# Kernel optimization log

Hardware: AMD Instinct MI355X
Metric: run time of the kernel (lower is better)

## Reference

```python
import jax, jax.numpy as jnp
import numpy as np

B, N, E = 4, 2048, 512
H, DK, DV = 8, 64, 64
QKV_OUT = H * (2 * DK + DV)  # 1536


def setup_inputs() -> dict:
    key = jax.random.key(0)
    ks = jax.random.split(key, 5)
    s_in = 1.0 / np.sqrt(E)
    s_o = 1.0 / np.sqrt(H * DV)
    x = jax.random.normal(ks[0], (B, N, E), dtype=jnp.float32)
    W_qkv = jax.random.uniform(ks[1], (E, QKV_OUT), jnp.float32, -s_in, s_in)
    b_qkv = jax.random.uniform(ks[2], (QKV_OUT,), jnp.float32, -s_in, s_in)
    W_o = jax.random.uniform(ks[3], (H * DV, E), jnp.float32, -s_o, s_o)
    b_o = jax.random.uniform(ks[4], (E,), jnp.float32, -s_o, s_o)
    return {"x": x, "W_qkv": W_qkv, "b_qkv": b_qkv, "W_o": W_o, "b_o": b_o}


def reference(x, W_qkv, b_qkv, W_o, b_o):
    scale = DK ** (-0.5)
    qkv = x @ W_qkv + b_qkv                      # [B, N, H*(2dk+dv)]
    # Faithful to torch: raw view (B, H, N, 2dk+dv), NOT a head-split transpose.
    qkv = qkv.reshape(B, H, N, 2 * DK + DV)
    q = qkv[..., :DK]
    k = qkv[..., DK:2 * DK]
    v = qkv[..., 2 * DK:]
    # Faithful bug: qk /= scale with scale = dk^-0.5 -> multiply by sqrt(dk).
    qk = jnp.einsum('bhnd,bhmd->bhnm', q, k) / scale   # [B, H, N, N]
    attn = jax.nn.softmax(qk, axis=-1)
    y = jnp.einsum('bhnm,bhmd->bhnd', attn, v)         # [B, H, N, dv]
    y = y.reshape(B, N, H * DV)
    return y @ W_o + b_o
```

## Files before the change

kernel.cpp:

```cpp
#include <hip/hip_runtime.h>
#include <hip/hip_bf16.h>
#include <math.h>


typedef __attribute__((ext_vector_type(8))) short bf16x8;
typedef __attribute__((ext_vector_type(4))) float f32x4;

#define MFMA16(a, b, c) __builtin_amdgcn_mfma_f32_16x16x32_bf16((a), (b), (c), 0, 0, 0)

__device__ __forceinline__ ushort f2bf_rne(float f) {
  union { float f; unsigned u; } v; v.f = f;
  return (ushort)((v.u + 0x7fffu + ((v.u >> 16) & 1u)) >> 16);
}
__device__ __forceinline__ float bf2f(ushort h) {
  union { float f; unsigned u; } v; v.u = ((unsigned)h) << 16; return v.f;
}
__device__ __forceinline__ void split2(float f, ushort& hi, ushort& lo) {
  union { float f; unsigned u; } v; v.f = f;
  hi = (ushort)(v.u >> 16);
  union { float f; unsigned u; } r; r.f = f - bf2f(hi);
  lo = (ushort)(r.u >> 16);
}

typedef __attribute__((address_space(3))) unsigned int lds_uint;
typedef const __attribute__((address_space(1))) unsigned int glob_uint;
__device__ __forceinline__ void gl_lds16(const ushort* g, short* l) {
  __builtin_amdgcn_global_load_lds((glob_uint*)g, (lds_uint*)l, 16, 0, 0);
}

template <bool ROOMY>
__global__ __launch_bounds__(256) void cvt_k(const float* __restrict__ wqkv,
                                             const float* __restrict__ wo,
                                             const float* __restrict__ x,
                                             ushort* __restrict__ wT_hi,
                                             ushort* __restrict__ wT_lo,
                                             ushort* __restrict__ woT,
                                             ushort* __restrict__ xh,
                                             ushort* __restrict__ xl)
{
  const int gid = blockIdx.x * 256 + threadIdx.x;
  if (gid < 786432) {
    const int c   = gid / 49152;
    const int rem = gid - c * 49152;
    const int n   = rem >> 5;
    const int k   = c * 32 + (rem & 31);
    ushort hi, lo; split2(wqkv[(size_t)k * 1536 + n], hi, lo);
    wT_hi[gid] = hi; wT_lo[gid] = lo;
  } else if (gid < 1048576) {
    const int g = gid - 786432;
    const int n = g >> 9, k = g & 511;
    woT[g] = f2bf_rne(wo[(size_t)k * 512 + n]);
  } else if (ROOMY) {
    const int g = gid - 1048576;
    float4 v = ((const float4*)x)[g];
    ushort4 hh, ll;
    split2(v.x, hh.x, ll.x); split2(v.y, hh.y, ll.y);
    split2(v.z, hh.z, ll.z); split2(v.w, hh.w, ll.w);
    ((ushort4*)xh)[g] = hh;
    ((ushort4*)xl)[g] = ll;
  }
}

template <bool PRECVT>
__global__ __launch_bounds__(256) void qkv_gemm_k(
    const float* __restrict__ x,
    const ushort* __restrict__ xh, const ushort* __restrict__ xl,
    const ushort* __restrict__ wT_hi, const ushort* __restrict__ wT_lo,
    const float* __restrict__ bqkv,
    ushort* __restrict__ q_hi, ushort* __restrict__ q_lo,
    ushort* __restrict__ k_hi, ushort* __restrict__ k_lo,
    ushort* __restrict__ v_nat)
{
  const int i = blockIdx.x, j = i >> 3;
  const int tmb = (i & 7) * 8 + (j & 7);
  const int tn  = j >> 3;
  const int tid = threadIdx.x, lane = tid & 63, w = tid >> 6;
  const int col16 = lane & 15, quad = lane >> 4;
  const int wr = w >> 1, wc = w & 1;

  __shared__ short sbuf[16384];

  const int wl   = w * 1024 + lane * 8;
  const int ldsw = w * 1024;
  const ushort* shp = wT_hi + (size_t)tn * 4096 + wl;
  const ushort* slp = wT_lo + (size_t)tn * 4096 + wl;

  const float*  axf[4];
  const ushort *axh[4], *axl[4];
#pragma unroll
  for (int rt = 0; rt < 4; ++rt) {
    const size_t rowoff = (size_t)(tmb * 128 + wr * 64 + rt * 16 + col16) * 512 + quad * 8;
    axf[rt] = x  + rowoff;
    axh[rt] = xh + rowoff;
    axl[rt] = xl + rowoff;
  }

  f32x4 acc[4][4];
#pragma unroll
  for (int rt = 0; rt < 4; ++rt)
#pragma unroll
    for (int ct = 0; ct < 4; ++ct) acc[rt][ct] = (f32x4){0.f, 0.f, 0.f, 0.f};

  gl_lds16(shp,       sbuf + ldsw);
  gl_lds16(shp + 512, sbuf + ldsw + 512);
  gl_lds16(slp,       sbuf + 8192 + ldsw);
  gl_lds16(slp + 512, sbuf + 8192 + ldsw + 512);
  __syncthreads();

  int buf = 0;
#pragma unroll
  for (int c = 0; c < 16; ++c) {
    if (c < 15) {
      const size_t co = (size_t)(c + 1) * 49152;
      const int nb = (buf ^ 1) * 4096;
      gl_lds16(shp + co,       sbuf + nb + ldsw);
      gl_lds16(shp + co + 512, sbuf + nb + ldsw + 512);
      gl_lds16(slp + co,       sbuf + 8192 + nb + ldsw);
      gl_lds16(slp + co + 512, sbuf + 8192 + nb + ldsw + 512);
    }
    const int k0 = c * 32;
    const short* bhb = sbuf + buf * 4096;
    const short* blb = sbuf + 8192 + buf * 4096;

    bf16x8 bh[4], bl[4];
#pragma unroll
    for (int ct = 0; ct < 4; ++ct) {
      const int roff = (wc * 64 + ct * 16 + col16) * 32 + quad * 8;
      bh[ct] = *(const bf16x8*)(bhb + roff);
      bl[ct] = *(const bf16x8*)(blb + roff);
    }
#pragma unroll
    for (int rt = 0; rt < 4; ++rt) {
      bf16x8 a_hi, a_lo;
      if constexpr (PRECVT) {
        a_hi = *(const bf16x8*)(axh[rt] + k0);
        a_lo = *(const bf16x8*)(axl[rt] + k0);
      } else {
        float4 xa = *(const float4*)(axf[rt] + k0);
        float4 xb = *(const float4*)(axf[rt] + k0 + 4);
#pragma unroll
        for (int jj = 0; jj < 4; ++jj) {
          ushort h, l;
          split2(((const float*)&xa)[jj], h, l);
          ((short*)&a_hi)[jj] = (short)h; ((short*)&a_lo)[jj] = (short)l;
          split2(((const float*)&xb)[jj], h, l);
          ((short*)&a_hi)[4 + jj] = (short)h; ((short*)&a_lo)[4 + jj] = (short)l;
        }
      }
#pragma unroll
      for (int ct = 0; ct < 4; ++ct) {
        acc[rt][ct] = MFMA16(a_hi, bh[ct], acc[rt][ct]);
        acc[rt][ct] = MFMA16(a_hi, bl[ct], acc[rt][ct]);
        acc[rt][ct] = MFMA16(a_lo, bh[ct], acc[rt][ct]);
      }
    }
    __syncthreads();
    buf ^= 1;
  }

  short* eph = sbuf + w * 2304;
  short* epl = eph + 1152;
  const int g0   = tn * 128 + wc * 64;
  const int sect = (g0 % 192) >> 6;
  const int s    = g0 / 192;
  float bv[4];
#pragma unroll
  for (int ct = 0; ct < 4; ++ct) bv[ct] = bqkv[g0 + ct * 16 + col16];

#pragma unroll
  for (int rt = 0; rt < 4; ++rt) {
#pragma unroll
    for (int ct = 0; ct < 4; ++ct) {
#pragma unroll
      for (int r = 0; r < 4; ++r) {
        const float val = acc[rt][ct][r] + bv[ct];
        const int o = (quad * 4 + r) * 72 + ct * 16 + col16;
        if (sect == 2) {
          eph[o] = (short)f2bf_rne(val);
        } else {
          ushort h, l; split2(val, h, l);
          eph[o] = (short)h; epl[o] = (short)l;
        }
      }
    }
#pragma unroll
    for (int p = 0; p < 2; ++p) {
      const int row = p * 8 + (lane >> 3);
      const int dsg = (lane & 7) * 8;
      const int grow = tmb * 128 + wr * 64 + rt * 16 + row;
      const int bhh = grow >> 8, a = grow & 255;
      const size_t idx = ((size_t)bhh * 2048 + 8 * a + s) * 64 + dsg;
      uint4 hv = *(const uint4*)(eph + row * 72 + dsg);
      if (sect == 0) {
        *(uint4*)(q_hi + idx) = hv;
        uint4 lv = *(const uint4*)(epl + row * 72 + dsg);
        *(uint4*)(q_lo + idx) = lv;
      } else if (sect == 1) {
        *(uint4*)(k_hi + idx) = hv;
        uint4 lv = *(const uint4*)(epl + row * 72 + dsg);
        *(uint4*)(k_lo + idx) = lv;
      } else {
        *(uint4*)(v_nat + idx) = hv;
      }
    }
  }
}

__global__ __launch_bounds__(256) void vtrans_k(const ushort* __restrict__ v_nat,
                                                ushort* __restrict__ vT)
{
  const int t  = blockIdx.x & 7;
  const int bh = blockIdx.x >> 3;
  const int tid = threadIdx.x;
  const int nl = tid & 63;
  const int dg = tid >> 6;
  const size_t base = (size_t)bh * 2048 * 64;
#pragma unroll
  for (int p = 0; p < 2; ++p) {
    const int dseg = dg + p * 4;
#pragma unroll
    for (int nb = 0; nb < 4; ++nb) {
      const int n = t * 256 + nb * 64 + nl;
      uint4 vv = *(const uint4*)(v_nat + base + (size_t)n * 64 + dseg * 8);
      const ushort* pv = (const ushort*)&vv;
#pragma unroll
      for (int j = 0; j < 8; ++j)
        vT[base + (size_t)(dseg * 8 + j) * 2048 + n] = pv[j];
    }
  }
}

__global__ __launch_bounds__(256, 2) void attn_k(
    const ushort* __restrict__ q_hi, const ushort* __restrict__ q_lo,
    const ushort* __restrict__ k_hi, const ushort* __restrict__ k_lo,
    const ushort* __restrict__ vT, ushort* __restrict__ y)
{
  const int i  = blockIdx.x;
  const int bh = (i & 7) * 4 + (i >> 7);
  const int qt = (i >> 3) & 15;
  const int tid = threadIdx.x, lane = tid & 63, w = tid >> 6;
  const int col16 = lane & 15, quad = lane >> 4;
  const int n7 = col16 & 7;

  __shared__ short sbuf[32768];

  const size_t base = (size_t)bh * 2048 * 64;
  const int qw = qt * 128 + w * 32;

  const ushort* khs = k_hi + base;
  const ushort* kls = k_lo + base;
  const ushort* vts = vT  + base;

  const int lrow = lane >> 3;
  const int lx8  = ((lane & 7) ^ lrow) * 8;

  bf16x8 qh[2][2], ql[2][2];
#pragma unroll
  for (int rf = 0; rf < 2; ++rf)
#pragma unroll
    for (int ks = 0; ks < 2; ++ks) {
      const size_t off = base + (size_t)(qw + rf * 16 + col16) * 64 + ks * 32 + quad * 8;
      qh[rf][ks] = *(const bf16x8*)(q_hi + off);
      ql[rf][ks] = *(const bf16x8*)(q_lo + off);
    }

  f32x4 oacc[2][4];
#pragma unroll
  for (int rf = 0; rf < 2; ++rf)
#pragma unroll
    for (int ct = 0; ct < 4; ++ct) oacc[rf][ct] = (f32x4){0.f, 0.f, 0.f, 0.f};
  f32x4 lsum[2] = {(f32x4){0.f, 0.f, 0.f, 0.f}, (f32x4){0.f, 0.f, 0.f, 0.f}};

  const float S2 = 11.541560327111707f;

  short* wp0 = sbuf + 24576 + w * 2048;

#define STAGE_CHUNK(cnext, nb)                                                \
  {                                                                           \
    _Pragma("unroll")                                                         \
    for (int ii = 0; ii < 6; ++ii) {                                          \
      const int ins = w * 6 + ii;                                             \
      const int plane = ins >> 3, sub = ins & 7;                              \
      short* dst = sbuf + ((nb) * 3 + plane) * 4096 + sub * 512;              \
      const ushort* src;                                                      \
      if (plane == 2)                                                         \
        src = vts + (size_t)(sub * 8 + lrow) * 2048 + (cnext) * 64 + lx8;     \
      else                                                                    \
        src = (plane ? kls : khs) + (cnext) * 4096 + sub * 512 + lrow * 64 + lx8; \
      gl_lds16(src, dst);                                                     \
    }                                                                         \
  }

  STAGE_CHUNK(0, 0);
  __syncthreads();

  int buf = 0;
  for (int c = 0; c < 32; ++c) {
    if (c < 31) STAGE_CHUNK(c + 1, buf ^ 1);

    const short* kb = sbuf + (buf * 3) * 4096;
    const short* lb = kb + 4096;
    const short* vb = kb + 8192;

    f32x4 sacc[2][4];
#pragma unroll
    for (int rf = 0; rf < 2; ++rf)
#pragma unroll
      for (int ct = 0; ct < 4; ++ct) sacc[rf][ct] = (f32x4){0.f, 0.f, 0.f, 0.f};

    __builtin_amdgcn_s_setprio(1);
#pragma unroll
    for (int ks = 0; ks < 2; ++ks) {
#pragma unroll
      for (int ct = 0; ct < 4; ++ct) {
        const int off = (ct * 16 + col16) * 64 + (((ks * 4 + quad) ^ n7) << 3);
        bf16x8 khf = *(const bf16x8*)(kb + off);
        bf16x8 klf = *(const bf16x8*)(lb + off);
#pragma unroll
        for (int rf = 0; rf < 2; ++rf) {
          sacc[rf][ct] = MFMA16(qh[rf][ks], khf, sacc[rf][ct]);
          sacc[rf][ct] = MFMA16(qh[rf][ks], klf, sacc[rf][ct]);
          sacc[rf][ct] = MFMA16(ql[rf][ks], khf, sacc[rf][ct]);
        }
      }
    }
    __builtin_amdgcn_s_setprio(0);

#pragma unroll
    for (int rf = 0; rf < 2; ++rf) {
#pragma unroll
      for (int ct = 0; ct < 4; ++ct) {
#pragma unroll
        for (int r = 0; r < 4; ++r) {
          const float p = __builtin_amdgcn_exp2f(fmaf(sacc[rf][ct][r], S2, -128.0f));
          union { float f; unsigned u; } pu; pu.f = p;
          union { unsigned u; float f; } pb; pb.u = pu.u & 0xffff0000u;
          lsum[rf][r] += pb.f;
          const int prow = quad * 4 + r;
          wp0[rf * 1024 + prow * 64 + ((ct * 16 + col16) ^ ((prow & 7) << 3))] =
              (short)(pu.u >> 16);
        }
      }
    }

    __builtin_amdgcn_s_setprio(1);
#pragma unroll
    for (int ks = 0; ks < 2; ++ks) {
#pragma unroll
      for (int ct = 0; ct < 4; ++ct) {
        const int voff = (ct * 16 + col16) * 64 + (((ks * 4 + quad) ^ n7) << 3);
        bf16x8 vv = *(const bf16x8*)(vb + voff);
        const int poff = col16 * 64 + (((ks * 4 + quad) ^ n7) << 3);
#pragma unroll
        for (int rf = 0; rf < 2; ++rf) {
          bf16x8 ap = *(const bf16x8*)(wp0 + rf * 1024 + poff);
          oacc[rf][ct] = MFMA16(ap, vv, oacc[rf][ct]);
        }
      }
    }
    __builtin_amdgcn_s_setprio(0);

    __syncthreads();
    buf ^= 1;
  }

#pragma unroll
  for (int rf = 0; rf < 2; ++rf) {
#pragma unroll
    for (int r = 0; r < 4; ++r) {
      float l = lsum[rf][r];
#pragma unroll
      for (int off = 1; off < 16; off <<= 1) l += __shfl_xor(l, off, 64);
      const float inv = 1.f / l;
      const int n = qw + rf * 16 + quad * 4 + r;
      const size_t orow = ((size_t)bh * 256 + (n >> 3)) * 512 + (n & 7) * 64;
#pragma unroll
      for (int ct = 0; ct < 4; ++ct)
        y[orow + ct * 16 + col16] = f2bf_rne(oacc[rf][ct][r] * inv);
    }
  }
#undef STAGE_CHUNK
}

__global__ __launch_bounds__(256) void out_gemm_k(
    const ushort* __restrict__ y, const ushort* __restrict__ woT,
    const float* __restrict__ bo, float* __restrict__ out)
{
  const int i = blockIdx.x, j = i >> 3;
  const int tmb = (i & 7) * 32 + (j & 31);
  const int tn  = j >> 5;
  const int tid = threadIdx.x, lane = tid & 63, w = tid >> 6;
  const int col16 = lane & 15, quad = lane >> 4;
  const int wr = w >> 1, wc = w & 1;

  __shared__ short b_lds[2][128][40];

  const int sn = tid >> 1, sk = (tid & 1) * 16;
  const ushort* bsrc = woT + (size_t)(tn * 128 + sn) * 512 + sk;

  const ushort* ay = y + (size_t)(tmb * 32 + wr * 16 + col16) * 512 + quad * 8;

  f32x4 acc[4];
#pragma unroll
  for (int ct = 0; ct < 4; ++ct) acc[ct] = (f32x4){0.f, 0.f, 0.f, 0.f};

  uint4 rb0 = *(const uint4*)(bsrc);
  uint4 rb1 = *(const uint4*)(bsrc + 8);
  *(uint4*)(&b_lds[0][sn][sk])     = rb0;
  *(uint4*)(&b_lds[0][sn][sk + 8]) = rb1;

  for (int c = 0; c < 16; ++c) {
    __syncthreads();
    if (c < 15) {
      const int k0 = (c + 1) * 32;
      rb0 = *(const uint4*)(bsrc + k0);
      rb1 = *(const uint4*)(bsrc + k0 + 8);
    }
    const int b = c & 1, k0 = c * 32;
    bf16x8 af = *(const bf16x8*)(ay + k0);
#pragma unroll
    for (int ct = 0; ct < 4; ++ct) {
      bf16x8 bfr = *(const bf16x8*)(&b_lds[b][wc * 64 + ct * 16 + col16][quad * 8]);
      acc[ct] = MFMA16(af, bfr, acc[ct]);
    }
    if (c < 15) {
      const int nb = b ^ 1;
      *(uint4*)(&b_lds[nb][sn][sk])     = rb0;
      *(uint4*)(&b_lds[nb][sn][sk + 8]) = rb1;
    }
  }
#pragma unroll
  for (int ct = 0; ct < 4; ++ct) {
    const int col = tn * 128 + wc * 64 + ct * 16 + col16;
    const float bval = bo[col];
#pragma unroll
    for (int r = 0; r < 4; ++r) {
      const int row = tmb * 32 + wr * 16 + quad * 4 + r;
      out[(size_t)row * 512 + col] = acc[ct][r] + bval;
    }
  }
}

extern "C" void kernel_launch(void* const* d_in, const int* in_sizes, int n_in,
                              void* d_out, int out_size, void* d_ws, size_t ws_size,
                              hipStream_t stream)
{
  const float* x    = (const float*)d_in[0];
  const float* Wqkv = (const float*)d_in[1];
  const float* bqkv = (const float*)d_in[2];
  const float* Wo   = (const float*)d_in[3];
  const float* bo   = (const float*)d_in[4];
  float* out = (float*)d_out;

  ushort* wT_hi = (ushort*)d_ws;
  ushort* wT_lo = wT_hi + 786432;
  ushort* woT   = wT_lo + 786432;
  ushort* q_hi  = woT   + 262144;
  ushort* q_lo  = q_hi  + 4194304;
  ushort* k_hi  = q_lo  + 4194304;
  ushort* k_lo  = k_hi  + 4194304;
  ushort* v_nat = k_lo  + 4194304;
  ushort* tail  = v_nat + 4194304;

  const bool roomy = ws_size >= 62390272ULL;
  ushort *xh, *xl, *vT, *y;
  if (roomy) {
    xh = tail; xl = tail + 4194304;
    vT = xh;   y  = xl;
  } else {
    xh = xl = nullptr;
    vT = tail; y = v_nat;
  }

  if (roomy) {
    cvt_k<true><<<8192, 256, 0, stream>>>(Wqkv, Wo, x, wT_hi, wT_lo, woT, xh, xl);
    qkv_gemm_k<true><<<768, 256, 0, stream>>>(x, xh, xl, wT_hi, wT_lo, bqkv,
                                              q_hi, q_lo, k_hi, k_lo, v_nat);
  } else {
    cvt_k<false><<<4096, 256, 0, stream>>>(Wqkv, Wo, x, wT_hi, wT_lo, woT,
                                           nullptr, nullptr);
    qkv_gemm_k<false><<<768, 256, 0, stream>>>(x, nullptr, nullptr, wT_hi, wT_lo,
                                               bqkv, q_hi, q_lo, k_hi, k_lo, v_nat);
  }
  vtrans_k<<<256, 256, 0, stream>>>(v_nat, vT);
  attn_k<<<512, 256, 0, stream>>>(q_hi, q_lo, k_hi, k_lo, vT, y);
  out_gemm_k<<<1024, 256, 0, stream>>>(y, woT, bo, out);
}
```

Before: 231.4 us.

## Split attention work across 8 waves with 16 query rows each

The attention kernel now launches 512 threads per block instead of 256, and each wave handles 16 query rows instead of 32. Staging work per wave is halved and per-wave register state (accumulators, Q fragments) shrinks, with launch bounds raised to target more resident waves. In exchange, each K/V fragment read from LDS feeds half as many MFMAs, so LDS read traffic per unit of compute doubles, and more waves contend at the per-chunk barrier.

```diff
diff --git a/kernel.cpp b/kernel.cpp
--- a/kernel.cpp
+++ b/kernel.cpp
@@ -230,7 +230,7 @@
   }
 }
 
-__global__ __launch_bounds__(256, 2) void attn_k(
+__global__ __launch_bounds__(512, 4) void attn_k(
     const ushort* __restrict__ q_hi, const ushort* __restrict__ q_lo,
     const ushort* __restrict__ k_hi, const ushort* __restrict__ k_lo,
     const ushort* __restrict__ vT, ushort* __restrict__ y)
@@ -245,7 +245,7 @@
   __shared__ short sbuf[32768];
 
   const size_t base = (size_t)bh * 2048 * 64;
-  const int qw = qt * 128 + w * 32;
+  const int qw = qt * 128 + w * 16;
 
   const ushort* khs = k_hi + base;
   const ushort* kls = k_lo + base;
@@ -254,32 +254,28 @@
   const int lrow = lane >> 3;
   const int lx8  = ((lane & 7) ^ lrow) * 8;
 
-  bf16x8 qh[2][2], ql[2][2];
-#pragma unroll
-  for (int rf = 0; rf < 2; ++rf)
-#pragma unroll
-    for (int ks = 0; ks < 2; ++ks) {
-      const size_t off = base + (size_t)(qw + rf * 16 + col16) * 64 + ks * 32 + quad * 8;
-      qh[rf][ks] = *(const bf16x8*)(q_hi + off);
-      ql[rf][ks] = *(const bf16x8*)(q_lo + off);
-    }
-
-  f32x4 oacc[2][4];
-#pragma unroll
-  for (int rf = 0; rf < 2; ++rf)
-#pragma unroll
-    for (int ct = 0; ct < 4; ++ct) oacc[rf][ct] = (f32x4){0.f, 0.f, 0.f, 0.f};
-  f32x4 lsum[2] = {(f32x4){0.f, 0.f, 0.f, 0.f}, (f32x4){0.f, 0.f, 0.f, 0.f}};
+  bf16x8 qh[2], ql[2];
+#pragma unroll
+  for (int ks = 0; ks < 2; ++ks) {
+    const size_t off = base + (size_t)(qw + col16) * 64 + ks * 32 + quad * 8;
+    qh[ks] = *(const bf16x8*)(q_hi + off);
+    ql[ks] = *(const bf16x8*)(q_lo + off);
+  }
+
+  f32x4 oacc[4];
+#pragma unroll
+  for (int ct = 0; ct < 4; ++ct) oacc[ct] = (f32x4){0.f, 0.f, 0.f, 0.f};
+  f32x4 lsum = (f32x4){0.f, 0.f, 0.f, 0.f};
 
   const float S2 = 11.541560327111707f;
 
-  short* wp0 = sbuf + 24576 + w * 2048;
+  short* wp0 = sbuf + 24576 + w * 1024;
 
 #define STAGE_CHUNK(cnext, nb)                                                \
   {                                                                           \
     _Pragma("unroll")                                                         \
-    for (int ii = 0; ii < 6; ++ii) {                                          \
-      const int ins = w * 6 + ii;                                             \
+    for (int ii = 0; ii < 3; ++ii) {                                          \
+      const int ins = w * 3 + ii;                                             \
       const int plane = ins >> 3, sub = ins & 7;                              \
       short* dst = sbuf + ((nb) * 3 + plane) * 4096 + sub * 512;              \
       const ushort* src;                                                      \
@@ -302,11 +298,9 @@
     const short* lb = kb + 4096;
     const short* vb = kb + 8192;
 
-    f32x4 sacc[2][4];
-#pragma unroll
-    for (int rf = 0; rf < 2; ++rf)
-#pragma unroll
-      for (int ct = 0; ct < 4; ++ct) sacc[rf][ct] = (f32x4){0.f, 0.f, 0.f, 0.f};
+    f32x4 sacc[4];
+#pragma unroll
+    for (int ct = 0; ct < 4; ++ct) sacc[ct] = (f32x4){0.f, 0.f, 0.f, 0.f};
 
     __builtin_amdgcn_s_setprio(1);
 #pragma unroll
@@ -316,30 +310,24 @@
         const int off = (ct * 16 + col16) * 64 + (((ks * 4 + quad) ^ n7) << 3);
         bf16x8 khf = *(const bf16x8*)(kb + off);
         bf16x8 klf = *(const bf16x8*)(lb + off);
-#pragma unroll
-        for (int rf = 0; rf < 2; ++rf) {
-          sacc[rf][ct] = MFMA16(qh[rf][ks], khf, sacc[rf][ct]);
-          sacc[rf][ct] = MFMA16(qh[rf][ks], klf, sacc[rf][ct]);
-          sacc[rf][ct] = MFMA16(ql[rf][ks], khf, sacc[rf][ct]);
-        }
+        sacc[ct] = MFMA16(qh[ks], khf, sacc[ct]);
+        sacc[ct] = MFMA16(qh[ks], klf, sacc[ct]);
+        sacc[ct] = MFMA16(ql[ks], khf, sacc[ct]);
       }
     }
     __builtin_amdgcn_s_setprio(0);
 
 #pragma unroll
-    for (int rf = 0; rf < 2; ++rf) {
-#pragma unroll
-      for (int ct = 0; ct < 4; ++ct) {
-#pragma unroll
-        for (int r = 0; r < 4; ++r) {
-          const float p = __builtin_amdgcn_exp2f(fmaf(sacc[rf][ct][r], S2, -128.0f));
-          union { float f; unsigned u; } pu; pu.f = p;
-          union { unsigned u; float f; } pb; pb.u = pu.u & 0xffff0000u;
-          lsum[rf][r] += pb.f;
-          const int prow = quad * 4 + r;
-          wp0[rf * 1024 + prow * 64 + ((ct * 16 + col16) ^ ((prow & 7) << 3))] =
-              (short)(pu.u >> 16);
-        }
+    for (int ct = 0; ct < 4; ++ct) {
+#pragma unroll
+      for (int r = 0; r < 4; ++r) {
+        const float p = __builtin_amdgcn_exp2f(fmaf(sacc[ct][r], S2, -128.0f));
+        union { float f; unsigned u; } pu; pu.f = p;
+        union { unsigned u; float f; } pb; pb.u = pu.u & 0xffff0000u;
+        lsum[r] += pb.f;
+        const int prow = quad * 4 + r;
+        wp0[prow * 64 + ((ct * 16 + col16) ^ ((prow & 7) << 3))] =
+            (short)(pu.u >> 16);
       }
     }
 
@@ -351,11 +339,8 @@
         const int voff = (ct * 16 + col16) * 64 + (((ks * 4 + quad) ^ n7) << 3);
         bf16x8 vv = *(const bf16x8*)(vb + voff);
         const int poff = col16 * 64 + (((ks * 4 + quad) ^ n7) << 3);
-#pragma unroll
-        for (int rf = 0; rf < 2; ++rf) {
-          bf16x8 ap = *(const bf16x8*)(wp0 + rf * 1024 + poff);
-          oacc[rf][ct] = MFMA16(ap, vv, oacc[rf][ct]);
-        }
+        bf16x8 ap = *(const bf16x8*)(wp0 + poff);
+        oacc[ct] = MFMA16(ap, vv, oacc[ct]);
       }
     }
     __builtin_amdgcn_s_setprio(0);
@@ -365,19 +350,16 @@
   }
 
 #pragma unroll
-  for (int rf = 0; rf < 2; ++rf) {
-#pragma unroll
-    for (int r = 0; r < 4; ++r) {
-      float l = lsum[rf][r];
-#pragma unroll
-      for (int off = 1; off < 16; off <<= 1) l += __shfl_xor(l, off, 64);
-      const float inv = 1.f / l;
-      const int n = qw + rf * 16 + quad * 4 + r;
-      const size_t orow = ((size_t)bh * 256 + (n >> 3)) * 512 + (n & 7) * 64;
-#pragma unroll
-      for (int ct = 0; ct < 4; ++ct)
-        y[orow + ct * 16 + col16] = f2bf_rne(oacc[rf][ct][r] * inv);
-    }
+  for (int r = 0; r < 4; ++r) {
+    float l = lsum[r];
+#pragma unroll
+    for (int off = 1; off < 16; off <<= 1) l += __shfl_xor(l, off, 64);
+    const float inv = 1.f / l;
+    const int n = qw + quad * 4 + r;
+    const size_t orow = ((size_t)bh * 256 + (n >> 3)) * 512 + (n & 7) * 64;
+#pragma unroll
+    for (int ct = 0; ct < 4; ++ct)
+      y[orow + ct * 16 + col16] = f2bf_rne(oacc[ct][r] * inv);
   }
 #undef STAGE_CHUNK
 }
@@ -483,6 +465,6 @@
                                                bqkv, q_hi, q_lo, k_hi, k_lo, v_nat);
   }
   vtrans_k<<<256, 256, 0, stream>>>(v_nat, vT);
-  attn_k<<<512, 256, 0, stream>>>(q_hi, q_lo, k_hi, k_lo, vT, y);
+  attn_k<<<512, 512, 0, stream>>>(q_hi, q_lo, k_hi, k_lo, vT, y);
   out_gemm_k<<<1024, 256, 0, stream>>>(y, woT, bo, out);
 }
```

Result: no change. 229.7 us (-0.7%).

## Split attention key chunk across two wave groups with LDS reduction

Applied to the files above, without the earlier changes.

Doubles the attention block to 512 threads, with each pair of waves sharing a query slice and splitting each 64-key chunk into two 32-key halves. Each wave computes its half of the scores and P·V partials, then the two halves are reduced through LDS at the end before normalization and store. The aim is more waves per CU to hide MFMA and LDS latency. In exchange it adds a final LDS reduction and barrier, and launch bounds now request higher occupancy, which may pressure registers.

```diff
diff --git a/kernel.cpp b/kernel.cpp
--- a/kernel.cpp
+++ b/kernel.cpp
@@ -230,7 +230,7 @@
   }
 }
 
-__global__ __launch_bounds__(256, 2) void attn_k(
+__global__ __launch_bounds__(512, 4) void attn_k(
     const ushort* __restrict__ q_hi, const ushort* __restrict__ q_lo,
     const ushort* __restrict__ k_hi, const ushort* __restrict__ k_lo,
     const ushort* __restrict__ vT, ushort* __restrict__ y)
@@ -239,13 +239,14 @@
   const int bh = (i & 7) * 4 + (i >> 7);
   const int qt = (i >> 3) & 15;
   const int tid = threadIdx.x, lane = tid & 63, w = tid >> 6;
+  const int qg = w & 3, kh2 = w >> 2;
   const int col16 = lane & 15, quad = lane >> 4;
   const int n7 = col16 & 7;
 
   __shared__ short sbuf[32768];
 
   const size_t base = (size_t)bh * 2048 * 64;
-  const int qw = qt * 128 + w * 32;
+  const int qw = qt * 128 + qg * 32;
 
   const ushort* khs = k_hi + base;
   const ushort* kls = k_lo + base;
@@ -273,13 +274,13 @@
 
   const float S2 = 11.541560327111707f;
 
-  short* wp0 = sbuf + 24576 + w * 2048;
+  short* wp0 = sbuf + 24576 + w * 1024;
 
 #define STAGE_CHUNK(cnext, nb)                                                \
   {                                                                           \
     _Pragma("unroll")                                                         \
-    for (int ii = 0; ii < 6; ++ii) {                                          \
-      const int ins = w * 6 + ii;                                             \
+    for (int ii = 0; ii < 3; ++ii) {                                          \
+      const int ins = w * 3 + ii;                                             \
       const int plane = ins >> 3, sub = ins & 7;                              \
       short* dst = sbuf + ((nb) * 3 + plane) * 4096 + sub * 512;              \
       const ushort* src;                                                      \
@@ -302,25 +303,26 @@
     const short* lb = kb + 4096;
     const short* vb = kb + 8192;
 
-    f32x4 sacc[2][4];
+    f32x4 sacc[2][2];
 #pragma unroll
     for (int rf = 0; rf < 2; ++rf)
 #pragma unroll
-      for (int ct = 0; ct < 4; ++ct) sacc[rf][ct] = (f32x4){0.f, 0.f, 0.f, 0.f};
+      for (int ctl = 0; ctl < 2; ++ctl) sacc[rf][ctl] = (f32x4){0.f, 0.f, 0.f, 0.f};
 
     __builtin_amdgcn_s_setprio(1);
 #pragma unroll
     for (int ks = 0; ks < 2; ++ks) {
 #pragma unroll
-      for (int ct = 0; ct < 4; ++ct) {
+      for (int ctl = 0; ctl < 2; ++ctl) {
+        const int ct = kh2 * 2 + ctl;
         const int off = (ct * 16 + col16) * 64 + (((ks * 4 + quad) ^ n7) << 3);
         bf16x8 khf = *(const bf16x8*)(kb + off);
         bf16x8 klf = *(const bf16x8*)(lb + off);
 #pragma unroll
         for (int rf = 0; rf < 2; ++rf) {
-          sacc[rf][ct] = MFMA16(qh[rf][ks], khf, sacc[rf][ct]);
-          sacc[rf][ct] = MFMA16(qh[rf][ks], klf, sacc[rf][ct]);
-          sacc[rf][ct] = MFMA16(ql[rf][ks], khf, sacc[rf][ct]);
+          sacc[rf][ctl] = MFMA16(qh[rf][ks], khf, sacc[rf][ctl]);
+          sacc[rf][ctl] = MFMA16(qh[rf][ks], klf, sacc[rf][ctl]);
+          sacc[rf][ctl] = MFMA16(ql[rf][ks], khf, sacc[rf][ctl]);
         }
       }
     }
@@ -329,15 +331,16 @@
 #pragma unroll
     for (int rf = 0; rf < 2; ++rf) {
 #pragma unroll
-      for (int ct = 0; ct < 4; ++ct) {
+      for (int ctl = 0; ctl < 2; ++ctl) {
 #pragma unroll
         for (int r = 0; r < 4; ++r) {
-          const float p = __builtin_amdgcn_exp2f(fmaf(sacc[rf][ct][r], S2, -128.0f));
+          const float p = __builtin_amdgcn_exp2f(fmaf(sacc[rf][ctl][r], S2, -128.0f));
           union { float f; unsigned u; } pu; pu.f = p;
           union { unsigned u; float f; } pb; pb.u = pu.u & 0xffff0000u;
           lsum[rf][r] += pb.f;
-          const int prow = quad * 4 + r;
-          wp0[rf * 1024 + prow * 64 + ((ct * 16 + col16) ^ ((prow & 7) << 3))] =
+          const int row = quad * 4 + r;
+          const int k   = ctl * 16 + col16;
+          wp0[rf * 512 + row * 32 + ((((k >> 3) ^ (row & 3))) << 3) + (k & 7)] =
               (short)(pu.u >> 16);
         }
       }
@@ -345,17 +348,14 @@
 
     __builtin_amdgcn_s_setprio(1);
 #pragma unroll
-    for (int ks = 0; ks < 2; ++ks) {
-#pragma unroll
-      for (int ct = 0; ct < 4; ++ct) {
-        const int voff = (ct * 16 + col16) * 64 + (((ks * 4 + quad) ^ n7) << 3);
+    for (int rf = 0; rf < 2; ++rf) {
+      bf16x8 ap = *(const bf16x8*)(wp0 + rf * 512 + col16 * 32 +
+                                   ((quad ^ (col16 & 3)) << 3));
+#pragma unroll
+      for (int ctd = 0; ctd < 4; ++ctd) {
+        const int voff = (ctd * 16 + col16) * 64 + (((kh2 * 4 + quad) ^ n7) << 3);
         bf16x8 vv = *(const bf16x8*)(vb + voff);
-        const int poff = col16 * 64 + (((ks * 4 + quad) ^ n7) << 3);
-#pragma unroll
-        for (int rf = 0; rf < 2; ++rf) {
-          bf16x8 ap = *(const bf16x8*)(wp0 + rf * 1024 + poff);
-          oacc[rf][ct] = MFMA16(ap, vv, oacc[rf][ct]);
-        }
+        oacc[rf][ctd] = MFMA16(ap, vv, oacc[rf][ctd]);
       }
     }
     __builtin_amdgcn_s_setprio(0);
@@ -365,18 +365,55 @@
   }
 
 #pragma unroll
-  for (int rf = 0; rf < 2; ++rf) {
+  for (int rf = 0; rf < 2; ++rf)
 #pragma unroll
     for (int r = 0; r < 4; ++r) {
       float l = lsum[rf][r];
 #pragma unroll
       for (int off = 1; off < 16; off <<= 1) l += __shfl_xor(l, off, 64);
-      const float inv = 1.f / l;
-      const int n = qw + rf * 16 + quad * 4 + r;
-      const size_t orow = ((size_t)bh * 256 + (n >> 3)) * 512 + (n & 7) * 64;
+      lsum[rf][r] = l;
+    }
+
+  float* fl = (float*)sbuf;
+  float* my = fl + (qg * 64 + lane) * 41;
+  if (kh2 == 1) {
+    int idx = 0;
+#pragma unroll
+    for (int rf = 0; rf < 2; ++rf)
 #pragma unroll
       for (int ct = 0; ct < 4; ++ct)
-        y[orow + ct * 16 + col16] = f2bf_rne(oacc[rf][ct][r] * inv);
+#pragma unroll
+        for (int r = 0; r < 4; ++r) my[idx++] = oacc[rf][ct][r];
+#pragma unroll
+    for (int rf = 0; rf < 2; ++rf)
+#pragma unroll
+      for (int r = 0; r < 4; ++r) my[idx++] = lsum[rf][r];
+  }
+  __syncthreads();
+  if (kh2 == 0) {
+    int idx = 0;
+#pragma unroll
+    for (int rf = 0; rf < 2; ++rf)
+#pragma unroll
+      for (int ct = 0; ct < 4; ++ct)
+#pragma unroll
+        for (int r = 0; r < 4; ++r) oacc[rf][ct][r] += my[idx++];
+#pragma unroll
+    for (int rf = 0; rf < 2; ++rf)
+#pragma unroll
+      for (int r = 0; r < 4; ++r) lsum[rf][r] += my[idx++];
+
+#pragma unroll
+    for (int rf = 0; rf < 2; ++rf) {
+#pragma unroll
+      for (int r = 0; r < 4; ++r) {
+        const float inv = 1.f / lsum[rf][r];
+        const int n = qw + rf * 16 + quad * 4 + r;
+        const size_t orow = ((size_t)bh * 256 + (n >> 3)) * 512 + (n & 7) * 64;
+#pragma unroll
+        for (int ct = 0; ct < 4; ++ct)
+          y[orow + ct * 16 + col16] = f2bf_rne(oacc[rf][ct][r] * inv);
+      }
     }
   }
 #undef STAGE_CHUNK
@@ -483,6 +520,6 @@
                                                bqkv, q_hi, q_lo, k_hi, k_lo, v_nat);
   }
   vtrans_k<<<256, 256, 0, stream>>>(v_nat, vT);
-  attn_k<<<512, 256, 0, stream>>>(q_hi, q_lo, k_hi, k_lo, vT, y);
+  attn_k<<<512, 512, 0, stream>>>(q_hi, q_lo, k_hi, k_lo, vT, y);
   out_gemm_k<<<1024, 256, 0, stream>>>(y, woT, bo, out);
 }
```

New measurement: 230.3 us. No clear change (-0.5%).
